# Kernel tuning notes

Measured on AMD Instinct MI355X. Metric: run time of the kernel, lower is better.

The kernel has to match this reference:

```python
import jax, jax.numpy as jnp
import numpy as np

N_NODES = 50000
N_EDGES = 600000
D_IN = 128
D_OUT = 128
P_DROP = 0.1
BN_EPS = 1e-5


def setup_inputs() -> dict:
    key = jax.random.key(0)
    ks = jax.random.split(key, 6)
    x = jax.random.normal(ks[0], (N_NODES, D_IN), dtype=jnp.float32)
    weight = jax.random.normal(ks[1], (D_IN, D_OUT), dtype=jnp.float32) * (1.0 / np.sqrt(D_IN))
    bias = jnp.zeros((D_OUT,), dtype=jnp.float32)
    gamma = jnp.ones((D_OUT,), dtype=jnp.float32)
    beta = jnp.zeros((D_OUT,), dtype=jnp.float32)
    dropout_u = jax.random.uniform(ks[2], (N_NODES, D_OUT), dtype=jnp.float32)
    edge_index = jax.random.randint(ks[3], (2, N_EDGES), 0, N_NODES, dtype=jnp.int64)
    return {"x": x, "weight": weight, "bias": bias, "gamma": gamma,
            "beta": beta, "dropout_u": dropout_u, "edge_index": edge_index}


def reference(x, weight, bias, gamma, beta, dropout_u, edge_index):
    N = x.shape[0]
    # --- GCNConv (add_self_loops=True, symmetric normalization) ---
    loop = jnp.arange(N, dtype=edge_index.dtype)
    src = jnp.concatenate([edge_index[0], loop])  # [E+N]
    dst = jnp.concatenate([edge_index[1], loop])  # [E+N]
    xw = x @ weight                               # [N, D_OUT] small GEMM
    deg = jnp.zeros((N,), dtype=xw.dtype).at[dst].add(1.0)
    dinv = jnp.where(deg > 0, jax.lax.rsqrt(jnp.maximum(deg, 1.0)), 0.0)
    norm = dinv[src] * dinv[dst]                  # [E+N]
    msgs = xw[src] * norm[:, None]                # gather: [E+N, D_OUT]
    z = jax.ops.segment_sum(msgs, dst, num_segments=N) + bias
    # --- activation -> BatchNorm (training stats) -> dropout ---
    z = jax.nn.relu(z)
    mean = jnp.mean(z, axis=0)
    var = jnp.mean((z - mean) ** 2, axis=0)       # biased var, as BN uses
    z = (z - mean) * jax.lax.rsqrt(var + BN_EPS) * gamma + beta
    keep = (dropout_u > P_DROP).astype(z.dtype)
    z = z * keep * (1.0 / (1.0 - P_DROP))
    return z.astype(x.dtype)
```

## Files before the change

### kernel.cpp

```cpp
#include <hip/hip_runtime.h>
#include <cstdint>
#include <cstddef>

#define D 128
#define P_DROP 0.1f
#define INV_KEEP (1.0f / 0.9f)
#define BN_EPS 1e-5f

typedef __attribute__((ext_vector_type(8))) short bf16x8;
typedef __attribute__((ext_vector_type(4))) float f32x4;

__device__ __forceinline__ unsigned f2bf(float f) {
    unsigned u = __float_as_uint(f);
    return (u + 0x7fffu + ((u >> 16) & 1u)) >> 16;
}
__device__ __forceinline__ float bf_lo(unsigned v) { return __uint_as_float(v << 16); }
__device__ __forceinline__ float bf_hi(unsigned v) { return __uint_as_float(v & 0xffff0000u); }

__global__ void k_init(float4* __restrict__ y4, int n4,
                       int* __restrict__ hist, int N,
                       float* __restrict__ bnacc,
                       int* __restrict__ ssrc, int* __restrict__ sdst, int E) {
    int stride = gridDim.x * blockDim.x;
    int i0 = blockIdx.x * blockDim.x + threadIdx.x;
    float4 z = make_float4(0.f, 0.f, 0.f, 0.f);
    for (int i = i0; i < n4; i += stride) y4[i] = z;
    for (int i = i0; i < N; i += stride) hist[i] = 0;
    if (i0 < 256) bnacc[i0] = 0.f;
    if (i0 < 64) { ssrc[E + i0] = 0; sdst[E + i0] = -1; }
}

__global__ void k_hist(const int* __restrict__ dst, int* __restrict__ hist, int E) {
    int i = blockIdx.x * blockDim.x + threadIdx.x;
    if (i < E) atomicAdd(&hist[dst[i]], 1);
}

__global__ void k_scanA(const int* __restrict__ hist, int* __restrict__ tmp,
                        int* __restrict__ blocksum, int N) {
    __shared__ int sd[256];
    int tid = threadIdx.x;
    int i = blockIdx.x * 256 + tid;
    sd[tid] = (i < N) ? hist[i] : 0;
    __syncthreads();
    for (int o = 1; o < 256; o <<= 1) {
        int t = (tid >= o) ? sd[tid - o] : 0;
        __syncthreads();
        sd[tid] += t;
        __syncthreads();
    }
    tmp[i] = sd[tid];
    if (tid == 255) blocksum[blockIdx.x] = sd[255];
}

__global__ void k_scanB(const int* __restrict__ blocksum, int* __restrict__ blockoff,
                        int NBLK) {
    __shared__ int sd[256];
    int tid = threadIdx.x;
    int v = (tid < NBLK) ? blocksum[tid] : 0;
    sd[tid] = v;
    __syncthreads();
    for (int o = 1; o < 256; o <<= 1) {
        int t = (tid >= o) ? sd[tid - o] : 0;
        __syncthreads();
        sd[tid] += t;
        __syncthreads();
    }
    if (tid < NBLK) blockoff[tid] = sd[tid] - v;
}

__global__ void k_scanC(const int* __restrict__ tmp, const int* __restrict__ blockoff,
                        const int* __restrict__ hist, int* __restrict__ cursor, int N) {
    int i = blockIdx.x * 256 + threadIdx.x;
    if (i < N) cursor[i] = tmp[i] + blockoff[blockIdx.x] - hist[i];
}

__global__ void k_place(const int* __restrict__ src, const int* __restrict__ dst,
                        int* __restrict__ cursor,
                        int* __restrict__ ssrc, int* __restrict__ sdst, int E) {
    int i = blockIdx.x * blockDim.x + threadIdx.x;
    if (i < E) {
        int d = dst[i];
        int p = atomicAdd(&cursor[d], 1);
        ssrc[p] = src[i];
        sdst[p] = d;
    }
}

__global__ __launch_bounds__(256) void k_gemm(
    const float* __restrict__ x, const float* __restrict__ w,
    const int* __restrict__ hist, unsigned short* __restrict__ xwb,
    float* __restrict__ dinv, int N) {
    __shared__ unsigned short xs[64][136];
    __shared__ unsigned short wt[128][136];
    int tid = threadIdx.x;
    int row0 = blockIdx.x * 64;

#pragma unroll
    for (int i = 0; i < 32; ++i) {
        int flat = tid + i * 256;
        int n = flat & 127;
        int kp = flat >> 7;
        float a0 = w[(size_t)(2 * kp) * D + n];
        float a1 = w[(size_t)(2 * kp + 1) * D + n];
        *(unsigned*)&wt[n][2 * kp] = f2bf(a0) | (f2bf(a1) << 16);
    }
#pragma unroll
    for (int i = 0; i < 8; ++i) {
        int flat = tid + i * 256;
        int r = flat >> 5;
        int kq = flat & 31;
        int row = row0 + r;
        float4 v = (row < N) ? *(const float4*)&x[(size_t)row * D + kq * 4]
                             : make_float4(0.f, 0.f, 0.f, 0.f);
        uint2 pk;
        pk.x = f2bf(v.x) | (f2bf(v.y) << 16);
        pk.y = f2bf(v.z) | (f2bf(v.w) << 16);
        *(uint2*)&xs[r][kq * 4] = pk;
    }
    __syncthreads();

    int wv = tid >> 6, lane = tid & 63;
    int l15 = lane & 15, quad = lane >> 4;
    int mrow = wv * 16 + l15;
    f32x4 acc[8];
#pragma unroll
    for (int t = 0; t < 8; ++t) acc[t] = (f32x4){0.f, 0.f, 0.f, 0.f};
#pragma unroll
    for (int k0 = 0; k0 < D; k0 += 32) {
        bf16x8 af = *(bf16x8*)&xs[mrow][k0 + quad * 8];
#pragma unroll
        for (int nt = 0; nt < 8; ++nt) {
            bf16x8 bfr = *(bf16x8*)&wt[nt * 16 + l15][k0 + quad * 8];
            acc[nt] = __builtin_amdgcn_mfma_f32_16x16x32_bf16(af, bfr, acc[nt], 0, 0, 0);
        }
    }
#pragma unroll
    for (int reg = 0; reg < 4; ++reg) {
        int node = row0 + wv * 16 + quad * 4 + reg;
        if (node < N) {
            float dv = rsqrtf((float)(hist[node] + 1));
            if (l15 == 0) dinv[node] = dv;
#pragma unroll
            for (int nt = 0; nt < 8; ++nt) {
                float val = acc[nt][reg] * dv;
                xwb[(size_t)node * D + nt * 16 + l15] = (unsigned short)f2bf(val);
            }
        }
    }
}

__global__ __launch_bounds__(256) void k_aggregate(
    const unsigned short* __restrict__ xwb, const float* __restrict__ dinv,
    const int* __restrict__ ssrc, const int* __restrict__ sdst,
    float* __restrict__ y, int E) {
    int lane = threadIdx.x & 63;
    int wv = threadIdx.x >> 6;
    int w = blockIdx.x * 4 + wv;
    int e0 = w * 64;
    if (e0 >= E) return;

    int vsrc = ssrc[e0 + lane];
    int vdst = sdst[e0 + lane];
    int prevd = (w > 0) ? __builtin_amdgcn_readfirstlane(sdst[e0 - 1]) : -5;
    int nextd = __builtin_amdgcn_readfirstlane(sdst[e0 + 64]);
    int cidx = vdst < 0 ? 0 : vdst;
    float dvv = dinv[cidx];

    float a0 = 0.f, a1 = 0.f;
    int cur = __builtin_amdgcn_readlane(vdst, 0);
    bool excl = (prevd != cur);

    unsigned vrow[32];
#pragma unroll
    for (int half = 0; half < 2; ++half) {
        int base = half * 32;
#pragma unroll
        for (int j = 0; j < 32; ++j) {
            int idx = __builtin_amdgcn_readlane(vsrc, base + j);
            vrow[j] = *(const unsigned*)(xwb + (size_t)idx * D + lane * 2);
        }
#pragma unroll
        for (int j = 0; j < 32; ++j) {
            int gj = base + j;
            int dj = __builtin_amdgcn_readlane(vdst, gj);
            if (dj != cur) {
                float dv = __int_as_float(
                    __builtin_amdgcn_readlane(__float_as_int(dvv), gj - 1));
                float s0 = a0 * dv, s1 = a1 * dv;
                float* yp = y + (size_t)cur * D + lane * 2;
                if (excl) { *(float2*)yp = make_float2(s0, s1); }
                else { atomicAdd(yp, s0); atomicAdd(yp + 1, s1); }
                a0 = 0.f; a1 = 0.f; cur = dj; excl = true;
            }
            unsigned v = vrow[j];
            a0 += bf_lo(v); a1 += bf_hi(v);
        }
    }
    if (cur >= 0) {
        float dv = __int_as_float(__builtin_amdgcn_readlane(__float_as_int(dvv), 63));
        float s0 = a0 * dv, s1 = a1 * dv;
        float* yp = y + (size_t)cur * D + lane * 2;
        if (excl && (nextd != cur)) { *(float2*)yp = make_float2(s0, s1); }
        else { atomicAdd(yp, s0); atomicAdd(yp + 1, s1); }
    }
}

__global__ __launch_bounds__(256) void k_postagg(
    float* __restrict__ y, const unsigned short* __restrict__ xwb,
    const float* __restrict__ dinv, const float* __restrict__ bias,
    float* __restrict__ bnacc, int total4) {
    int tid = threadIdx.x;
    int stride = gridDim.x * 256;
    int c4 = tid & 31;
    float4 b4 = ((const float4*)bias)[c4];
    float s0 = 0.f, s1 = 0.f, s2 = 0.f, s3 = 0.f;
    float q0 = 0.f, q1 = 0.f, q2 = 0.f, q3 = 0.f;
    for (int i = blockIdx.x * 256 + tid; i < total4; i += stride) {
        int node = i >> 5;
        float4 z = ((float4*)y)[i];
        uint2 sv = *(const uint2*)(xwb + (size_t)node * D + c4 * 4);
        float dv = dinv[node];
        z.x = fmaxf(fmaf(bf_lo(sv.x), dv, z.x) + b4.x, 0.f);
        z.y = fmaxf(fmaf(bf_hi(sv.x), dv, z.y) + b4.y, 0.f);
        z.z = fmaxf(fmaf(bf_lo(sv.y), dv, z.z) + b4.z, 0.f);
        z.w = fmaxf(fmaf(bf_hi(sv.y), dv, z.w) + b4.w, 0.f);
        ((float4*)y)[i] = z;
        s0 += z.x; s1 += z.y; s2 += z.z; s3 += z.w;
        q0 += z.x * z.x; q1 += z.y * z.y; q2 += z.z * z.z; q3 += z.w * z.w;
    }
    __shared__ float red[256][8];
    red[tid][0] = s0; red[tid][1] = s1; red[tid][2] = s2; red[tid][3] = s3;
    red[tid][4] = q0; red[tid][5] = q1; red[tid][6] = q2; red[tid][7] = q3;
    __syncthreads();
    if (tid < 128) {
        int r0 = tid >> 2, sl = tid & 3;
        float acc = 0.f;
#pragma unroll
        for (int m = 0; m < 8; ++m) acc += red[r0 + 32 * m][sl];
        atomicAdd(&bnacc[tid], acc);
    } else {
        int t = tid - 128;
        int r0 = t >> 2, sl = 4 + (t & 3);
        float acc = 0.f;
#pragma unroll
        for (int m = 0; m < 8; ++m) acc += red[r0 + 32 * m][sl];
        atomicAdd(&bnacc[128 + t], acc);
    }
}

__global__ void k_bnfinal(const float* __restrict__ bnacc, const float* __restrict__ gamma,
                          const float* __restrict__ beta, float* __restrict__ scsh, int N) {
    int c = threadIdx.x;
    if (c < 128) {
        float invN = 1.0f / (float)N;
        float mean = bnacc[c] * invN;
        float var = bnacc[128 + c] * invN - mean * mean;
        var = fmaxf(var, 0.f);
        float sc = gamma[c] * rsqrtf(var + BN_EPS);
        scsh[c] = sc;
        scsh[128 + c] = beta[c] - mean * sc;
    }
}

__global__ __launch_bounds__(256) void k_finalize(
    float* __restrict__ out, const float* __restrict__ u,
    const float* __restrict__ scsh, int total4) {
    int i = blockIdx.x * 256 + threadIdx.x;
    if (i >= total4) return;
    float4 v = ((const float4*)out)[i];
    float4 uu = ((const float4*)u)[i];
    int c = (i & 31) * 4;
    float s0 = scsh[c], s1 = scsh[c + 1], s2 = scsh[c + 2], s3 = scsh[c + 3];
    float h0 = scsh[128 + c], h1 = scsh[128 + c + 1];
    float h2 = scsh[128 + c + 2], h3 = scsh[128 + c + 3];
    v.x = fmaf(v.x, s0, h0) * (uu.x > P_DROP ? INV_KEEP : 0.f);
    v.y = fmaf(v.y, s1, h1) * (uu.y > P_DROP ? INV_KEEP : 0.f);
    v.z = fmaf(v.z, s2, h2) * (uu.z > P_DROP ? INV_KEEP : 0.f);
    v.w = fmaf(v.w, s3, h3) * (uu.w > P_DROP ? INV_KEEP : 0.f);
    ((float4*)out)[i] = v;
}

extern "C" void kernel_launch(void* const* d_in, const int* in_sizes, int n_in,
                              void* d_out, int out_size, void* d_ws, size_t ws_size,
                              hipStream_t stream) {
    const float* x      = (const float*)d_in[0];
    const float* weight = (const float*)d_in[1];
    const float* bias   = (const float*)d_in[2];
    const float* gamma  = (const float*)d_in[3];
    const float* beta   = (const float*)d_in[4];
    const float* du     = (const float*)d_in[5];
    const int*   eidx   = (const int*)d_in[6];
    float* out = (float*)d_out;

    const int N = in_sizes[0] / D;
    const int E = in_sizes[6] / 2;
    const int* esrc = eidx;
    const int* edst = eidx + E;

    char* p = (char*)d_ws;
    auto alloc = [&](size_t bytes) {
        char* q = p;
        p += (bytes + 255) & ~(size_t)255;
        return q;
    };
    unsigned short* xwb = (unsigned short*)alloc((size_t)N * D * sizeof(unsigned short));
    int*   hist     = (int*)alloc((size_t)N * sizeof(int));
    int*   cursor   = (int*)alloc((size_t)N * sizeof(int));
    const int NBLK = (N + 255) / 256;
    int*   tmp      = (int*)alloc((size_t)NBLK * 256 * sizeof(int));
    int*   blocksum = (int*)alloc((size_t)NBLK * sizeof(int));
    int*   blockoff = (int*)alloc((size_t)NBLK * sizeof(int));
    int*   ssrc     = (int*)alloc((size_t)(E + 64) * sizeof(int));
    int*   sdst     = (int*)alloc((size_t)(E + 64) * sizeof(int));
    float* dinv     = (float*)alloc((size_t)N * sizeof(float));
    float* bnacc    = (float*)alloc(256 * sizeof(float));
    float* scsh     = (float*)alloc(256 * sizeof(float));

    const int EB = (E + 255) / 256;
    const int total4 = N * (D / 4);
    hipLaunchKernelGGL(k_init, dim3(1024), dim3(256), 0, stream,
                       (float4*)out, total4, hist, N, bnacc, ssrc, sdst, E);
    hipLaunchKernelGGL(k_hist, dim3(EB), dim3(256), 0, stream, edst, hist, E);
    hipLaunchKernelGGL(k_scanA, dim3(NBLK), dim3(256), 0, stream, hist, tmp, blocksum, N);
    hipLaunchKernelGGL(k_scanB, dim3(1), dim3(256), 0, stream, blocksum, blockoff, NBLK);
    hipLaunchKernelGGL(k_scanC, dim3(NBLK), dim3(256), 0, stream, tmp, blockoff, hist, cursor, N);
    hipLaunchKernelGGL(k_place, dim3(EB), dim3(256), 0, stream, esrc, edst, cursor, ssrc, sdst, E);
    hipLaunchKernelGGL(k_gemm, dim3((N + 63) / 64), dim3(256), 0, stream,
                       x, weight, hist, xwb, dinv, N);
    const int NWAVE = (E + 63) / 64;
    hipLaunchKernelGGL(k_aggregate, dim3((NWAVE + 3) / 4), dim3(256), 0, stream,
                       xwb, dinv, ssrc, sdst, out, E);
    hipLaunchKernelGGL(k_postagg, dim3(1024), dim3(256), 0, stream,
                       out, xwb, dinv, bias, bnacc, total4);
    hipLaunchKernelGGL(k_bnfinal, dim3(1), dim3(128), 0, stream, bnacc, gamma, beta, scsh, N);
    hipLaunchKernelGGL(k_finalize, dim3((total4 + 255) / 256), dim3(256), 0, stream,
                       out, du, scsh, total4);
}
```

Measured before the change: 256.0 us.

## Switch to CSR per-node aggregation with fused bias/ReLU/BN stats, drop atomics

Replaces the edge-sorted segmented aggregation, which used atomics and a zeroed output, with a CSR pull scheme. Each wave owns one destination node and walks its neighbour list, padded to a multiple of 8 with a dummy zero row. The self-loop, bias, ReLU and BatchNorm statistics are fused into the aggregation, and the BN finalize is folded into the dropout kernel. The scan kernels are merged and the sdst array and the output zeroing pass are removed. In exchange, the padded edge array adds memory traffic, and one wave per node may underuse lanes on low-degree nodes and load-balance poorly.

```diff
diff --git a/kernel.cpp b/kernel.cpp
--- a/kernel.cpp
+++ b/kernel.cpp
@@ -17,17 +17,16 @@
 __device__ __forceinline__ float bf_lo(unsigned v) { return __uint_as_float(v << 16); }
 __device__ __forceinline__ float bf_hi(unsigned v) { return __uint_as_float(v & 0xffff0000u); }
 
-__global__ void k_init(float4* __restrict__ y4, int n4,
-                       int* __restrict__ hist, int N,
+__global__ void k_init(int* __restrict__ hist, int N,
                        float* __restrict__ bnacc,
-                       int* __restrict__ ssrc, int* __restrict__ sdst, int E) {
+                       int* __restrict__ ssrc, int PS,
+                       unsigned short* __restrict__ xwb) {
     int stride = gridDim.x * blockDim.x;
     int i0 = blockIdx.x * blockDim.x + threadIdx.x;
-    float4 z = make_float4(0.f, 0.f, 0.f, 0.f);
-    for (int i = i0; i < n4; i += stride) y4[i] = z;
+    for (int i = i0; i < PS; i += stride) ssrc[i] = N;
     for (int i = i0; i < N; i += stride) hist[i] = 0;
     if (i0 < 256) bnacc[i0] = 0.f;
-    if (i0 < 64) { ssrc[E + i0] = 0; sdst[E + i0] = -1; }
+    if (i0 < 64) ((unsigned*)(xwb + (size_t)N * D))[i0] = 0u;
 }
 
 __global__ void k_hist(const int* __restrict__ dst, int* __restrict__ hist, int E) {
@@ -40,7 +39,7 @@
     __shared__ int sd[256];
     int tid = threadIdx.x;
     int i = blockIdx.x * 256 + tid;
-    sd[tid] = (i < N) ? hist[i] : 0;
+    sd[tid] = (i < N) ? ((hist[i] + 7) & ~7) : 0;
     __syncthreads();
     for (int o = 1; o < 256; o <<= 1) {
         int t = (tid >= o) ? sd[tid - o] : 0;
@@ -52,37 +51,36 @@
     if (tid == 255) blocksum[blockIdx.x] = sd[255];
 }
 
-__global__ void k_scanB(const int* __restrict__ blocksum, int* __restrict__ blockoff,
-                        int NBLK) {
+__global__ void k_scanBC(const int* __restrict__ tmp, const int* __restrict__ blocksum,
+                         const int* __restrict__ hist,
+                         int* __restrict__ rowptr, int* __restrict__ cursor,
+                         int N, int NBLK) {
     __shared__ int sd[256];
     int tid = threadIdx.x;
-    int v = (tid < NBLK) ? blocksum[tid] : 0;
-    sd[tid] = v;
-    __syncthreads();
-    for (int o = 1; o < 256; o <<= 1) {
-        int t = (tid >= o) ? sd[tid - o] : 0;
+    int b = blockIdx.x;
+    sd[tid] = (tid < NBLK && tid < b) ? blocksum[tid] : 0;
+    __syncthreads();
+    for (int o = 128; o > 0; o >>= 1) {
+        if (tid < o) sd[tid] += sd[tid + o];
         __syncthreads();
-        sd[tid] += t;
-        __syncthreads();
-    }
-    if (tid < NBLK) blockoff[tid] = sd[tid] - v;
-}
-
-__global__ void k_scanC(const int* __restrict__ tmp, const int* __restrict__ blockoff,
-                        const int* __restrict__ hist, int* __restrict__ cursor, int N) {
-    int i = blockIdx.x * 256 + threadIdx.x;
-    if (i < N) cursor[i] = tmp[i] + blockoff[blockIdx.x] - hist[i];
+    }
+    int boff = sd[0];
+    int i = b * 256 + tid;
+    if (i < N) {
+        int pd = (hist[i] + 7) & ~7;
+        int r = tmp[i] + boff - pd;
+        rowptr[i] = r;
+        cursor[i] = r;
+    }
 }
 
 __global__ void k_place(const int* __restrict__ src, const int* __restrict__ dst,
-                        int* __restrict__ cursor,
-                        int* __restrict__ ssrc, int* __restrict__ sdst, int E) {
+                        int* __restrict__ cursor, int* __restrict__ ssrc, int E) {
     int i = blockIdx.x * blockDim.x + threadIdx.x;
     if (i < E) {
         int d = dst[i];
         int p = atomicAdd(&cursor[d], 1);
         ssrc[p] = src[i];
-        sdst[p] = d;
     }
 }
 
@@ -151,133 +149,83 @@
 
 __global__ __launch_bounds__(256) void k_aggregate(
     const unsigned short* __restrict__ xwb, const float* __restrict__ dinv,
-    const int* __restrict__ ssrc, const int* __restrict__ sdst,
-    float* __restrict__ y, int E) {
-    int lane = threadIdx.x & 63;
-    int wv = threadIdx.x >> 6;
-    int w = blockIdx.x * 4 + wv;
-    int e0 = w * 64;
-    if (e0 >= E) return;
-
-    int vsrc = ssrc[e0 + lane];
-    int vdst = sdst[e0 + lane];
-    int prevd = (w > 0) ? __builtin_amdgcn_readfirstlane(sdst[e0 - 1]) : -5;
-    int nextd = __builtin_amdgcn_readfirstlane(sdst[e0 + 64]);
-    int cidx = vdst < 0 ? 0 : vdst;
-    float dvv = dinv[cidx];
-
-    float a0 = 0.f, a1 = 0.f;
-    int cur = __builtin_amdgcn_readlane(vdst, 0);
-    bool excl = (prevd != cur);
-
-    unsigned vrow[32];
-#pragma unroll
-    for (int half = 0; half < 2; ++half) {
-        int base = half * 32;
-#pragma unroll
-        for (int j = 0; j < 32; ++j) {
-            int idx = __builtin_amdgcn_readlane(vsrc, base + j);
-            vrow[j] = *(const unsigned*)(xwb + (size_t)idx * D + lane * 2);
+    const int* __restrict__ ssrc, const int* __restrict__ rowptr,
+    const int* __restrict__ hist, const float* __restrict__ bias,
+    float* __restrict__ y, float* __restrict__ bnacc, int N) {
+    int tid = threadIdx.x;
+    int lane = tid & 63;
+    int wv = tid >> 6;
+    int w0 = blockIdx.x * 4 + wv;
+    int totw = gridDim.x * 4;
+    float2 b2 = *(const float2*)(bias + lane * 2);
+    float s0 = 0.f, s1 = 0.f, q0 = 0.f, q1 = 0.f;
+
+    for (int n = w0; n < N; n += totw) {
+        int nn = __builtin_amdgcn_readfirstlane(n);
+        int base = rowptr[nn];
+        int deg = hist[nn];
+        int pdeg = (deg + 7) & ~7;
+        unsigned sv = *(const unsigned*)(xwb + (size_t)nn * D + lane * 2);
+        float a0 = bf_lo(sv), a1 = bf_hi(sv);
+
+        for (int c0 = 0; c0 < pdeg; c0 += 64) {
+            int vsrc = ssrc[base + c0 + lane];
+            int lim = min(64, pdeg - c0);
+            for (int j0 = 0; j0 < lim; j0 += 8) {
+                unsigned vr[8];
+#pragma unroll
+                for (int j = 0; j < 8; ++j) {
+                    int idx = __builtin_amdgcn_readlane(vsrc, j0 + j);
+                    vr[j] = *(const unsigned*)(xwb + (size_t)idx * D + lane * 2);
+                }
+#pragma unroll
+                for (int j = 0; j < 8; ++j) { a0 += bf_lo(vr[j]); a1 += bf_hi(vr[j]); }
+            }
         }
-#pragma unroll
-        for (int j = 0; j < 32; ++j) {
-            int gj = base + j;
-            int dj = __builtin_amdgcn_readlane(vdst, gj);
-            if (dj != cur) {
-                float dv = __int_as_float(
-                    __builtin_amdgcn_readlane(__float_as_int(dvv), gj - 1));
-                float s0 = a0 * dv, s1 = a1 * dv;
-                float* yp = y + (size_t)cur * D + lane * 2;
-                if (excl) { *(float2*)yp = make_float2(s0, s1); }
-                else { atomicAdd(yp, s0); atomicAdd(yp + 1, s1); }
-                a0 = 0.f; a1 = 0.f; cur = dj; excl = true;
-            }
-            unsigned v = vrow[j];
-            a0 += bf_lo(v); a1 += bf_hi(v);
-        }
-    }
-    if (cur >= 0) {
-        float dv = __int_as_float(__builtin_amdgcn_readlane(__float_as_int(dvv), 63));
-        float s0 = a0 * dv, s1 = a1 * dv;
-        float* yp = y + (size_t)cur * D + lane * 2;
-        if (excl && (nextd != cur)) { *(float2*)yp = make_float2(s0, s1); }
-        else { atomicAdd(yp, s0); atomicAdd(yp + 1, s1); }
-    }
-}
-
-__global__ __launch_bounds__(256) void k_postagg(
-    float* __restrict__ y, const unsigned short* __restrict__ xwb,
-    const float* __restrict__ dinv, const float* __restrict__ bias,
-    float* __restrict__ bnacc, int total4) {
-    int tid = threadIdx.x;
-    int stride = gridDim.x * 256;
-    int c4 = tid & 31;
-    float4 b4 = ((const float4*)bias)[c4];
-    float s0 = 0.f, s1 = 0.f, s2 = 0.f, s3 = 0.f;
-    float q0 = 0.f, q1 = 0.f, q2 = 0.f, q3 = 0.f;
-    for (int i = blockIdx.x * 256 + tid; i < total4; i += stride) {
-        int node = i >> 5;
-        float4 z = ((float4*)y)[i];
-        uint2 sv = *(const uint2*)(xwb + (size_t)node * D + c4 * 4);
-        float dv = dinv[node];
-        z.x = fmaxf(fmaf(bf_lo(sv.x), dv, z.x) + b4.x, 0.f);
-        z.y = fmaxf(fmaf(bf_hi(sv.x), dv, z.y) + b4.y, 0.f);
-        z.z = fmaxf(fmaf(bf_lo(sv.y), dv, z.z) + b4.z, 0.f);
-        z.w = fmaxf(fmaf(bf_hi(sv.y), dv, z.w) + b4.w, 0.f);
-        ((float4*)y)[i] = z;
-        s0 += z.x; s1 += z.y; s2 += z.z; s3 += z.w;
-        q0 += z.x * z.x; q1 += z.y * z.y; q2 += z.z * z.z; q3 += z.w * z.w;
-    }
-    __shared__ float red[256][8];
-    red[tid][0] = s0; red[tid][1] = s1; red[tid][2] = s2; red[tid][3] = s3;
-    red[tid][4] = q0; red[tid][5] = q1; red[tid][6] = q2; red[tid][7] = q3;
-    __syncthreads();
-    if (tid < 128) {
-        int r0 = tid >> 2, sl = tid & 3;
-        float acc = 0.f;
-#pragma unroll
-        for (int m = 0; m < 8; ++m) acc += red[r0 + 32 * m][sl];
-        atomicAdd(&bnacc[tid], acc);
-    } else {
-        int t = tid - 128;
-        int r0 = t >> 2, sl = 4 + (t & 3);
-        float acc = 0.f;
-#pragma unroll
-        for (int m = 0; m < 8; ++m) acc += red[r0 + 32 * m][sl];
-        atomicAdd(&bnacc[128 + t], acc);
-    }
-}
-
-__global__ void k_bnfinal(const float* __restrict__ bnacc, const float* __restrict__ gamma,
-                          const float* __restrict__ beta, float* __restrict__ scsh, int N) {
-    int c = threadIdx.x;
-    if (c < 128) {
-        float invN = 1.0f / (float)N;
-        float mean = bnacc[c] * invN;
-        float var = bnacc[128 + c] * invN - mean * mean;
-        var = fmaxf(var, 0.f);
-        float sc = gamma[c] * rsqrtf(var + BN_EPS);
-        scsh[c] = sc;
-        scsh[128 + c] = beta[c] - mean * sc;
-    }
+        float dv = dinv[nn];
+        float z0 = fmaxf(fmaf(a0, dv, b2.x), 0.f);
+        float z1 = fmaxf(fmaf(a1, dv, b2.y), 0.f);
+        *(float2*)(y + (size_t)nn * D + lane * 2) = make_float2(z0, z1);
+        s0 += z0; s1 += z1; q0 += z0 * z0; q1 += z1 * z1;
+    }
+
+    __shared__ float red[256][4];
+    red[tid][0] = s0; red[tid][1] = s1; red[tid][2] = q0; red[tid][3] = q1;
+    __syncthreads();
+    int o = tid;
+    int col = o & 127;
+    int l = col >> 1;
+    int si = ((o >= 128) ? 2 : 0) + (col & 1);
+    float acc = red[0 * 64 + l][si] + red[1 * 64 + l][si] +
+                red[2 * 64 + l][si] + red[3 * 64 + l][si];
+    atomicAdd(&bnacc[o], acc);
 }
 
 __global__ __launch_bounds__(256) void k_finalize(
     float* __restrict__ out, const float* __restrict__ u,
-    const float* __restrict__ scsh, int total4) {
-    int i = blockIdx.x * 256 + threadIdx.x;
-    if (i >= total4) return;
-    float4 v = ((const float4*)out)[i];
-    float4 uu = ((const float4*)u)[i];
-    int c = (i & 31) * 4;
-    float s0 = scsh[c], s1 = scsh[c + 1], s2 = scsh[c + 2], s3 = scsh[c + 3];
-    float h0 = scsh[128 + c], h1 = scsh[128 + c + 1];
-    float h2 = scsh[128 + c + 2], h3 = scsh[128 + c + 3];
-    v.x = fmaf(v.x, s0, h0) * (uu.x > P_DROP ? INV_KEEP : 0.f);
-    v.y = fmaf(v.y, s1, h1) * (uu.y > P_DROP ? INV_KEEP : 0.f);
-    v.z = fmaf(v.z, s2, h2) * (uu.z > P_DROP ? INV_KEEP : 0.f);
-    v.w = fmaf(v.w, s3, h3) * (uu.w > P_DROP ? INV_KEEP : 0.f);
-    ((float4*)out)[i] = v;
+    const float* __restrict__ bnacc, const float* __restrict__ gamma,
+    const float* __restrict__ beta, int total4, float invN) {
+    __shared__ float sc[128], sh[128];
+    int tid = threadIdx.x;
+    if (tid < 128) {
+        float mean = bnacc[tid] * invN;
+        float var = fmaxf(bnacc[128 + tid] * invN - mean * mean, 0.f);
+        float s = gamma[tid] * rsqrtf(var + BN_EPS);
+        sc[tid] = s;
+        sh[tid] = beta[tid] - mean * s;
+    }
+    __syncthreads();
+    int stride = gridDim.x * 256;
+    for (int i = blockIdx.x * 256 + tid; i < total4; i += stride) {
+        float4 v = ((const float4*)out)[i];
+        float4 uu = ((const float4*)u)[i];
+        int c = (i & 31) * 4;
+        v.x = fmaf(v.x, sc[c],     sh[c])     * (uu.x > P_DROP ? INV_KEEP : 0.f);
+        v.y = fmaf(v.y, sc[c + 1], sh[c + 1]) * (uu.y > P_DROP ? INV_KEEP : 0.f);
+        v.z = fmaf(v.z, sc[c + 2], sh[c + 2]) * (uu.z > P_DROP ? INV_KEEP : 0.f);
+        v.w = fmaf(v.w, sc[c + 3], sh[c + 3]) * (uu.w > P_DROP ? INV_KEEP : 0.f);
+        ((float4*)out)[i] = v;
+    }
 }
 
 extern "C" void kernel_launch(void* const* d_in, const int* in_sizes, int n_in,
@@ -303,36 +251,32 @@
         p += (bytes + 255) & ~(size_t)255;
         return q;
     };
-    unsigned short* xwb = (unsigned short*)alloc((size_t)N * D * sizeof(unsigned short));
+    unsigned short* xwb = (unsigned short*)alloc((size_t)(N + 1) * D * sizeof(unsigned short));
     int*   hist     = (int*)alloc((size_t)N * sizeof(int));
     int*   cursor   = (int*)alloc((size_t)N * sizeof(int));
+    int*   rowptr   = (int*)alloc((size_t)N * sizeof(int));
     const int NBLK = (N + 255) / 256;
     int*   tmp      = (int*)alloc((size_t)NBLK * 256 * sizeof(int));
     int*   blocksum = (int*)alloc((size_t)NBLK * sizeof(int));
-    int*   blockoff = (int*)alloc((size_t)NBLK * sizeof(int));
-    int*   ssrc     = (int*)alloc((size_t)(E + 64) * sizeof(int));
-    int*   sdst     = (int*)alloc((size_t)(E + 64) * sizeof(int));
+    const int PS = E + 7 * N + 64;
+    int*   ssrc     = (int*)alloc((size_t)PS * sizeof(int));
     float* dinv     = (float*)alloc((size_t)N * sizeof(float));
     float* bnacc    = (float*)alloc(256 * sizeof(float));
-    float* scsh     = (float*)alloc(256 * sizeof(float));
 
     const int EB = (E + 255) / 256;
     const int total4 = N * (D / 4);
+
     hipLaunchKernelGGL(k_init, dim3(1024), dim3(256), 0, stream,
-                       (float4*)out, total4, hist, N, bnacc, ssrc, sdst, E);
+                       hist, N, bnacc, ssrc, PS, xwb);
     hipLaunchKernelGGL(k_hist, dim3(EB), dim3(256), 0, stream, edst, hist, E);
     hipLaunchKernelGGL(k_scanA, dim3(NBLK), dim3(256), 0, stream, hist, tmp, blocksum, N);
-    hipLaunchKernelGGL(k_scanB, dim3(1), dim3(256), 0, stream, blocksum, blockoff, NBLK);
-    hipLaunchKernelGGL(k_scanC, dim3(NBLK), dim3(256), 0, stream, tmp, blockoff, hist, cursor, N);
-    hipLaunchKernelGGL(k_place, dim3(EB), dim3(256), 0, stream, esrc, edst, cursor, ssrc, sdst, E);
+    hipLaunchKernelGGL(k_scanBC, dim3(NBLK), dim3(256), 0, stream,
+                       tmp, blocksum, hist, rowptr, cursor, N, NBLK);
+    hipLaunchKernelGGL(k_place, dim3(EB), dim3(256), 0, stream, esrc, edst, cursor, ssrc, E);
     hipLaunchKernelGGL(k_gemm, dim3((N + 63) / 64), dim3(256), 0, stream,
                        x, weight, hist, xwb, dinv, N);
-    const int NWAVE = (E + 63) / 64;
-    hipLaunchKernelGGL(k_aggregate, dim3((NWAVE + 3) / 4), dim3(256), 0, stream,
-                       xwb, dinv, ssrc, sdst, out, E);
-    hipLaunchKernelGGL(k_postagg, dim3(1024), dim3(256), 0, stream,
-                       out, xwb, dinv, bias, bnacc, total4);
-    hipLaunchKernelGGL(k_bnfinal, dim3(1), dim3(128), 0, stream, bnacc, gamma, beta, scsh, N);
-    hipLaunchKernelGGL(k_finalize, dim3((total4 + 255) / 256), dim3(256), 0, stream,
-                       out, du, scsh, total4);
-}
+    hipLaunchKernelGGL(k_aggregate, dim3(1024), dim3(256), 0, stream,
+                       xwb, dinv, ssrc, rowptr, hist, bias, out, bnacc, N);
+    hipLaunchKernelGGL(k_finalize, dim3(2048), dim3(256), 0, stream,
+                       out, du, bnacc, gamma, beta, total4, 1.0f / (float)N);
+}
```

Measured after the change: 238.0 us. -7.0%, faster.
